# Kernel tuning notes

Hardware: AMD Instinct MI355X
Metric: run time of the kernel (lower is better)

Reference implementation:

```python
import jax, jax.numpy as jnp
import numpy as np
from math import log

X_SIZE, Y_SIZE, W_SIZE = 512, 512, 256
SIGMA = 2.0
TIME_CONST = 1000.0 / log(SIGMA)  # default time_constant = 1000/log(sigma)


def setup_inputs() -> dict:
    key = jax.random.key(0)
    k1, k2 = jax.random.split(key)
    x = jax.random.normal(k1, (W_SIZE,), dtype=jnp.float32)
    W = jax.random.normal(k2, (X_SIZE, Y_SIZE, W_SIZE), dtype=jnp.float32)
    return {"x": x, "W": W, "time_step": 100}


def reference(x, W, time_step):
    # per-cell L2 distance: (X_SIZE, Y_SIZE)
    d = jnp.linalg.norm(x - W, ord=2, axis=-1)
    flat = jnp.argmin(d)
    wx, wy = jnp.unravel_index(flat, (X_SIZE, Y_SIZE))
    # torch.meshgrid default 'ij' indexing
    GX, GY = jnp.meshgrid(
        jnp.arange(X_SIZE, dtype=jnp.float32),
        jnp.arange(Y_SIZE, dtype=jnp.float32),
        indexing="ij",
    )
    decay = SIGMA * jnp.exp(-jnp.float32(time_step) / TIME_CONST)
    denom = 2.0 * decay * decay
    # Faithful to torch: GX.T[wx, wy] == wy and GY.T[wx, wy] == wx
    distx = (GX - wy.astype(jnp.float32)) ** 2
    disty = (GY - wx.astype(jnp.float32)) ** 2
    h = (jnp.exp(-distx / denom) * jnp.exp(-disty / denom)).T
    return h, (wx, wy)
```

## Files before the change

kernel.cpp:

```cpp
#include <hip/hip_runtime.h>
#include <math.h>

#define XS 512
#define YS 512
#define WDIM 256
#define NCELLS (XS * YS)
#define K1_BLOCKS 2048
#define K1_THREADS 256
#define NSLOTS 32
#define SLOT_STRIDE 16

typedef float vfloat4 __attribute__((ext_vector_type(4)));

__global__ __launch_bounds__(K1_THREADS) void som_dist_kernel(
    const float* __restrict__ x,
    const float* __restrict__ W,
    unsigned long long* __restrict__ ws) {
  const int lane = threadIdx.x & 63;
  const int waveInBlock = threadIdx.x >> 6;
  const int gw = blockIdx.x * (K1_THREADS / 64) + waveInBlock;

  const vfloat4 xv = ((const vfloat4*)x)[lane];

  float bestD = 3.4e38f;
  int bestI = 0;

  const int base = gw * 32;
  const int r7 = lane & 7;

  const bool b0 = (lane & 1) != 0;
  const bool b1 = (lane & 2) != 0;
  const bool b2 = (lane & 4) != 0;

  vfloat4 buf[2][8];

  {
    const vfloat4* p0 = (const vfloat4*)(W + (size_t)base * WDIM) + lane;
#pragma unroll
    for (int r = 0; r < 8; ++r)
      buf[0][r] = __builtin_nontemporal_load(p0 + r * (WDIM / 4));
  }

#pragma unroll
  for (int b = 0; b < 4; ++b) {
    if (b < 3) {
      const vfloat4* pn =
          (const vfloat4*)(W + (size_t)(base + (b + 1) * 8) * WDIM) + lane;
#pragma unroll
      for (int r = 0; r < 8; ++r)
        buf[(b + 1) & 1][r] = __builtin_nontemporal_load(pn + r * (WDIM / 4));
    }

    const int cb = base + b * 8;
    float s[8];
#pragma unroll
    for (int r = 0; r < 8; ++r) {
      const vfloat4 wv = buf[b & 1][r];
      const float dx = xv.x - wv.x;
      const float dy = xv.y - wv.y;
      const float dz = xv.z - wv.z;
      const float dw = xv.w - wv.w;
      s[r] = dx * dx + dy * dy + dz * dz + dw * dw;
    }

    float t0, t1, t2, t3;
    {
      float k, sd;
      k = b0 ? s[1] : s[0]; sd = b0 ? s[0] : s[1];
      t0 = k + __shfl_xor(sd, 1, 64);
      k = b0 ? s[3] : s[2]; sd = b0 ? s[2] : s[3];
      t1 = k + __shfl_xor(sd, 1, 64);
      k = b0 ? s[5] : s[4]; sd = b0 ? s[4] : s[5];
      t2 = k + __shfl_xor(sd, 1, 64);
      k = b0 ? s[7] : s[6]; sd = b0 ? s[6] : s[7];
      t3 = k + __shfl_xor(sd, 1, 64);
    }
    float u0, u1;
    {
      float k, sd;
      k = b1 ? t1 : t0; sd = b1 ? t0 : t1;
      u0 = k + __shfl_xor(sd, 2, 64);
      k = b1 ? t3 : t2; sd = b1 ? t2 : t3;
      u1 = k + __shfl_xor(sd, 2, 64);
    }
    float v;
    {
      const float k = b2 ? u1 : u0;
      const float sd = b2 ? u0 : u1;
      v = k + __shfl_xor(sd, 4, 64);
    }
    v += __shfl_xor(v, 8, 64);
    v += __shfl_xor(v, 16, 64);
    v += __shfl_xor(v, 32, 64);

    if (v < bestD) { bestD = v; bestI = cb + r7; }
  }

  unsigned long long packed =
      ((unsigned long long)__float_as_uint(bestD) << 32) | (unsigned int)bestI;

#pragma unroll
  for (int off = 32; off > 0; off >>= 1) {
    const unsigned long long o = __shfl_xor(packed, off, 64);
    packed = (o < packed) ? o : packed;
  }

  __shared__ unsigned long long sbest[K1_THREADS / 64];
  if (lane == 0) sbest[waveInBlock] = packed;
  __syncthreads();
  if (threadIdx.x == 0) {
    unsigned long long m = sbest[0];
#pragma unroll
    for (int i = 1; i < K1_THREADS / 64; ++i) {
      const unsigned long long v2 = sbest[i];
      m = (v2 < m) ? v2 : m;
    }
    atomicMin(ws + (blockIdx.x & (NSLOTS - 1)) * SLOT_STRIDE, m);
  }
}

__global__ __launch_bounds__(256) void som_h_kernel(
    const unsigned long long* __restrict__ ws,
    const int* __restrict__ time_step,
    float* __restrict__ out) {
  const int t = threadIdx.x;
  const int lane = t & 63;

  unsigned long long v = ws[(lane & (NSLOTS - 1)) * SLOT_STRIDE];
#pragma unroll
  for (int off = 1; off < 32; off <<= 1) {
    const unsigned long long o = __shfl_xor(v, off, 64);
    v = (o < v) ? o : v;
  }

  const int flat = (int)(v & 0xFFFFFFFFULL);
  const int wx = flat >> 9;
  const int wy = flat & (YS - 1);

  const float ts = (float)(*time_step);
  const float TIME_CONST = 1442.6950408889634f;
  const float decay = 2.0f * expf(-ts / TIME_CONST);
  const float denom = 2.0f * decay * decay;
  const float inv = -1.0f / denom;

  const int e = blockIdx.x * 1024 + t * 4;
  const int i = e >> 9;
  const int j0 = e & (YS - 1);
  const float di = (float)(i - wx);
  const float di2 = di * di;

  const float d0 = (float)(j0 + 0 - wy);
  const float d1 = (float)(j0 + 1 - wy);
  const float d2 = (float)(j0 + 2 - wy);
  const float d3 = (float)(j0 + 3 - wy);
  vfloat4 r;
  r.x = expf((di2 + d0 * d0) * inv);
  r.y = expf((di2 + d1 * d1) * inv);
  r.z = expf((di2 + d2 * d2) * inv);
  r.w = expf((di2 + d3 * d3) * inv);
  ((vfloat4*)out)[e >> 2] = r;

  if (blockIdx.x == 0 && t == 0) {
    out[NCELLS] = (float)wx;
    out[NCELLS + 1] = (float)wy;
  }
}

extern "C" void kernel_launch(void* const* d_in, const int* in_sizes, int n_in,
                              void* d_out, int out_size, void* d_ws, size_t ws_size,
                              hipStream_t stream) {
  const float* x = (const float*)d_in[0];
  const float* W = (const float*)d_in[1];
  const int* ts = (const int*)d_in[2];
  float* out = (float*)d_out;
  unsigned long long* ws = (unsigned long long*)d_ws;

  (void)hipMemsetAsync(ws, 0xFF, NSLOTS * SLOT_STRIDE * 8, stream);
  som_dist_kernel<<<K1_BLOCKS, K1_THREADS, 0, stream>>>(x, W, ws);
  som_h_kernel<<<NCELLS / 1024, 256, 0, stream>>>(ws, ts, out);
}
```

Before: 339.8 us.

## Issue all W loads up front with grid-strided mapping and transposed shuffle reduction

Each thread now issues all 32 of its float4 loads of W at once. The loads are strided by the total thread count, so one wave handles 32 cells spread across the whole W array instead of 32 adjacent cells. This replaces the double-buffered nontemporal batches of 8 rows. The partial sums are then reduced with a full 5-level transposed butterfly, which leaves lane i holding the distance of iteration i. The aim is more memory-level parallelism and fewer shuffle rounds, at the cost of higher register pressure and dropping the nontemporal hint.

```diff
diff --git a/kernel.cpp b/kernel.cpp
--- a/kernel.cpp
+++ b/kernel.cpp
@@ -7,6 +7,9 @@
 #define NCELLS (XS * YS)
 #define K1_BLOCKS 2048
 #define K1_THREADS 256
+#define NTHREADS (K1_BLOCKS * K1_THREADS)
+#define NWAVES (NTHREADS / 64)
+#define K1_ITERS 32
 #define NSLOTS 32
 #define SLOT_STRIDE 16
 
@@ -16,88 +19,67 @@
     const float* __restrict__ x,
     const float* __restrict__ W,
     unsigned long long* __restrict__ ws) {
-  const int lane = threadIdx.x & 63;
-  const int waveInBlock = threadIdx.x >> 6;
-  const int gw = blockIdx.x * (K1_THREADS / 64) + waveInBlock;
+  const int tid = threadIdx.x;
+  const int lane = tid & 63;
+  const int waveInBlock = tid >> 6;
+  const int gtid = blockIdx.x * K1_THREADS + tid;
+  const int w = gtid >> 6;
 
   const vfloat4 xv = ((const vfloat4*)x)[lane];
+  const vfloat4* __restrict__ W4 = (const vfloat4*)W;
 
-  float bestD = 3.4e38f;
-  int bestI = 0;
-
-  const int base = gw * 32;
-  const int r7 = lane & 7;
+  float acc[K1_ITERS];
+#pragma unroll
+  for (int it = 0; it < K1_ITERS; ++it) {
+    const vfloat4 v = W4[(size_t)gtid + (size_t)it * NTHREADS];
+    const float dx = xv.x - v.x;
+    const float dy = xv.y - v.y;
+    const float dz = xv.z - v.z;
+    const float dw = xv.w - v.w;
+    acc[it] = dx * dx + dy * dy + dz * dz + dw * dw;
+  }
 
   const bool b0 = (lane & 1) != 0;
   const bool b1 = (lane & 2) != 0;
   const bool b2 = (lane & 4) != 0;
-
-  vfloat4 buf[2][8];
-
-  {
-    const vfloat4* p0 = (const vfloat4*)(W + (size_t)base * WDIM) + lane;
-#pragma unroll
-    for (int r = 0; r < 8; ++r)
-      buf[0][r] = __builtin_nontemporal_load(p0 + r * (WDIM / 4));
-  }
+  const bool b3 = (lane & 8) != 0;
+  const bool b4 = (lane & 16) != 0;
 
 #pragma unroll
-  for (int b = 0; b < 4; ++b) {
-    if (b < 3) {
-      const vfloat4* pn =
-          (const vfloat4*)(W + (size_t)(base + (b + 1) * 8) * WDIM) + lane;
+  for (int j = 0; j < 16; ++j) {
+    const float keep = b0 ? acc[2 * j + 1] : acc[2 * j];
+    const float send = b0 ? acc[2 * j] : acc[2 * j + 1];
+    acc[j] = keep + __shfl_xor(send, 1, 64);
+  }
 #pragma unroll
-      for (int r = 0; r < 8; ++r)
-        buf[(b + 1) & 1][r] = __builtin_nontemporal_load(pn + r * (WDIM / 4));
-    }
+  for (int j = 0; j < 8; ++j) {
+    const float keep = b1 ? acc[2 * j + 1] : acc[2 * j];
+    const float send = b1 ? acc[2 * j] : acc[2 * j + 1];
+    acc[j] = keep + __shfl_xor(send, 2, 64);
+  }
+#pragma unroll
+  for (int j = 0; j < 4; ++j) {
+    const float keep = b2 ? acc[2 * j + 1] : acc[2 * j];
+    const float send = b2 ? acc[2 * j] : acc[2 * j + 1];
+    acc[j] = keep + __shfl_xor(send, 4, 64);
+  }
+#pragma unroll
+  for (int j = 0; j < 2; ++j) {
+    const float keep = b3 ? acc[2 * j + 1] : acc[2 * j];
+    const float send = b3 ? acc[2 * j] : acc[2 * j + 1];
+    acc[j] = keep + __shfl_xor(send, 8, 64);
+  }
+  {
+    const float keep = b4 ? acc[1] : acc[0];
+    const float send = b4 ? acc[0] : acc[1];
+    acc[0] = keep + __shfl_xor(send, 16, 64);
+  }
+  const float v = acc[0] + __shfl_xor(acc[0], 32, 64);
 
-    const int cb = base + b * 8;
-    float s[8];
-#pragma unroll
-    for (int r = 0; r < 8; ++r) {
-      const vfloat4 wv = buf[b & 1][r];
-      const float dx = xv.x - wv.x;
-      const float dy = xv.y - wv.y;
-      const float dz = xv.z - wv.z;
-      const float dw = xv.w - wv.w;
-      s[r] = dx * dx + dy * dy + dz * dz + dw * dw;
-    }
-
-    float t0, t1, t2, t3;
-    {
-      float k, sd;
-      k = b0 ? s[1] : s[0]; sd = b0 ? s[0] : s[1];
-      t0 = k + __shfl_xor(sd, 1, 64);
-      k = b0 ? s[3] : s[2]; sd = b0 ? s[2] : s[3];
-      t1 = k + __shfl_xor(sd, 1, 64);
-      k = b0 ? s[5] : s[4]; sd = b0 ? s[4] : s[5];
-      t2 = k + __shfl_xor(sd, 1, 64);
-      k = b0 ? s[7] : s[6]; sd = b0 ? s[6] : s[7];
-      t3 = k + __shfl_xor(sd, 1, 64);
-    }
-    float u0, u1;
-    {
-      float k, sd;
-      k = b1 ? t1 : t0; sd = b1 ? t0 : t1;
-      u0 = k + __shfl_xor(sd, 2, 64);
-      k = b1 ? t3 : t2; sd = b1 ? t2 : t3;
-      u1 = k + __shfl_xor(sd, 2, 64);
-    }
-    float v;
-    {
-      const float k = b2 ? u1 : u0;
-      const float sd = b2 ? u0 : u1;
-      v = k + __shfl_xor(sd, 4, 64);
-    }
-    v += __shfl_xor(v, 8, 64);
-    v += __shfl_xor(v, 16, 64);
-    v += __shfl_xor(v, 32, 64);
-
-    if (v < bestD) { bestD = v; bestI = cb + r7; }
-  }
+  const int cell = w + (lane & 31) * NWAVES;
 
   unsigned long long packed =
-      ((unsigned long long)__float_as_uint(bestD) << 32) | (unsigned int)bestI;
+      ((unsigned long long)__float_as_uint(v) << 32) | (unsigned int)cell;
 
 #pragma unroll
   for (int off = 32; off > 0; off >>= 1) {
@@ -108,7 +90,7 @@
   __shared__ unsigned long long sbest[K1_THREADS / 64];
   if (lane == 0) sbest[waveInBlock] = packed;
   __syncthreads();
-  if (threadIdx.x == 0) {
+  if (tid == 0) {
     unsigned long long m = sbest[0];
 #pragma unroll
     for (int i = 1; i < K1_THREADS / 64; ++i) {
```

Result: slower. 375.0 us (+10.4%).
